# Performance work log

Hardware: AMD Instinct MI355X
Metric: run time of the kernel (lower is better)

The kernel has to match this reference:

```python
import jax, jax.numpy as jnp
import numpy as np

N, E_EDGES = 100000, 1600000
IN_DIM, HEADS, OUT_DIM = 128, 8, 8


def setup_inputs() -> dict:
    key = jax.random.key(0)
    ks = jax.random.split(key, 12)
    d = HEADS * OUT_DIM
    s = 1.0 / np.sqrt(IN_DIM)
    inp = {
        'x': jax.random.normal(ks[0], (N, IN_DIM), dtype=jnp.float32),
        'edge_attr': jax.random.normal(ks[1], (E_EDGES, 1), dtype=jnp.float32),
        'edge_index': jax.random.randint(ks[2], (2, E_EDGES), 0, N, dtype=jnp.int64),
        'Wq': jax.random.normal(ks[3], (IN_DIM, d), dtype=jnp.float32) * s,
        'bq': jnp.zeros((d,), dtype=jnp.float32),
        'Wk': jax.random.normal(ks[4], (IN_DIM, d), dtype=jnp.float32) * s,
        'bk': jnp.zeros((d,), dtype=jnp.float32),
        'We': jax.random.normal(ks[5], (1, d), dtype=jnp.float32),
        'be': jnp.zeros((d,), dtype=jnp.float32),
        'Wv': jax.random.normal(ks[6], (IN_DIM, d), dtype=jnp.float32) * s,
        'bv': jnp.zeros((d,), dtype=jnp.float32),
    }
    return inp


def reference(x, edge_attr, edge_index, Wq, bq, Wk, bk, We, be, Wv, bv):
    n = x.shape[0]
    # Projections, reshaped to [N, H, D] (and [E, H, D] for edge features)
    Qh = (x @ Wq + bq).reshape(n, HEADS, OUT_DIM)
    Kh = (x @ Wk + bk).reshape(n, HEADS, OUT_DIM)
    Vh = (x @ Wv + bv).reshape(n, HEADS, OUT_DIM)
    Eh = (edge_attr @ We + be).reshape(-1, HEADS, OUT_DIM)

    src = edge_index[0]
    dst = edge_index[1]
    # Per-edge score: (K[src] * Q[dst] / sqrt(D)) * E, summed over D, clamped, exp'd
    score = (Kh[src] * Qh[dst]) * (1.0 / np.sqrt(OUT_DIM)) * Eh  # [E, H, D]
    score = jnp.exp(jnp.clip(jnp.sum(score, axis=-1, keepdims=True), -5.0, 5.0))  # [E, H, 1]

    msg = Vh[src] * score  # [E, H, D]
    wV = jax.ops.segment_sum(msg, dst, num_segments=n)     # [N, H, D]
    Z = jax.ops.segment_sum(score, dst, num_segments=n)    # [N, H, 1]
    return wV / (Z + 1e-6)
```

## Files before the change

kernel.cpp:

```cpp
#include <hip/hip_runtime.h>
#include <math.h>

#define NN 100000
#define EE 1600000
#define IND 128
#define D64 64

#define BSHIFT 8
#define NBUCK 391
#define P1_TILE 3072
#define NB_P1 521

typedef __attribute__((ext_vector_type(8))) short  short8;
typedef __attribute__((ext_vector_type(4))) float  f32x4;

__device__ __forceinline__ unsigned short bf16_rne(float v) {
    unsigned int u = __float_as_uint(v);
    return (unsigned short)((u + 0x7FFFu + ((u >> 16) & 1u)) >> 16);
}

__global__ __launch_bounds__(256) void wtrans_kernel(
    const float* __restrict__ Wq, const float* __restrict__ Wk,
    const float* __restrict__ Wv,
    unsigned short* __restrict__ wt_hi, unsigned short* __restrict__ wt_lo)
{
    int idx = blockIdx.x * 256 + threadIdx.x;
    if (idx >= 192 * 128) return;
    int col = idx >> 7, k = idx & 127;
    const float* W = (col < 64) ? Wq : (col < 128) ? Wk : Wv;
    float v = W[(size_t)k * D64 + (col & 63)];
    unsigned short h = bf16_rne(v);
    float hf = __uint_as_float((unsigned int)h << 16);
    unsigned short l = bf16_rne(v - hf);
    wt_hi[idx] = h;
    wt_lo[idx] = l;
}

#define XP 132

__global__ __launch_bounds__(256) void qkv_kernel(
    const float* __restrict__ x,
    const unsigned short* __restrict__ wt_hi,
    const unsigned short* __restrict__ wt_lo,
    const float* __restrict__ bq, const float* __restrict__ bk,
    const float* __restrict__ bv,
    float* __restrict__ Qo, unsigned int* __restrict__ KVb)
{
    __shared__ unsigned short xhi[32 * XP];
    __shared__ unsigned short xlo[32 * XP];

    const int t    = threadIdx.x;
    const int wave = t >> 6;
    const int lane = t & 63;
    const int nb   = blockIdx.x * 32;

    {
        const int row = t >> 3;
        const int c   = t & 7;
        const float* xr = x + (size_t)(nb + row) * IND + c * 16;
        float4 a0 = *(const float4*)(xr);
        float4 a1 = *(const float4*)(xr + 4);
        float4 a2 = *(const float4*)(xr + 8);
        float4 a3 = *(const float4*)(xr + 12);
        float vs[16] = { a0.x, a0.y, a0.z, a0.w, a1.x, a1.y, a1.z, a1.w,
                         a2.x, a2.y, a2.z, a2.w, a3.x, a3.y, a3.z, a3.w };
        short8 h0, h1, l0, l1;
#pragma unroll
        for (int j = 0; j < 8; ++j) {
            unsigned short hb = bf16_rne(vs[j]);
            float hf = __uint_as_float((unsigned int)hb << 16);
            h0[j] = (short)hb;
            l0[j] = (short)bf16_rne(vs[j] - hf);
        }
#pragma unroll
        for (int j = 0; j < 8; ++j) {
            unsigned short hb = bf16_rne(vs[8 + j]);
            float hf = __uint_as_float((unsigned int)hb << 16);
            h1[j] = (short)hb;
            l1[j] = (short)bf16_rne(vs[8 + j] - hf);
        }
        int o0 = row * XP + c * 16;
        *(short8*)&xhi[o0]     = h0;
        *(short8*)&xhi[o0 + 8] = h1;
        *(short8*)&xlo[o0]     = l0;
        *(short8*)&xlo[o0 + 8] = l1;
    }
    __syncthreads();

    const int wcol0 = wave * 48;

    f32x4 acc[2][3];
#pragma unroll
    for (int rt = 0; rt < 2; ++rt)
#pragma unroll
        for (int ct = 0; ct < 3; ++ct)
            acc[rt][ct] = (f32x4){0.f, 0.f, 0.f, 0.f};

#pragma unroll
    for (int kt = 0; kt < 4; ++kt) {
        short8 bh[3], bl[3];
#pragma unroll
        for (int ct = 0; ct < 3; ++ct) {
            int col = wcol0 + ct * 16 + (lane & 15);
            int a = col * 128 + kt * 32 + (lane >> 4) * 8;
            bh[ct] = *(const short8*)&wt_hi[a];
            bl[ct] = *(const short8*)&wt_lo[a];
        }
        short8 ah[2], al[2];
#pragma unroll
        for (int rt = 0; rt < 2; ++rt) {
            int o2 = (rt * 16 + (lane & 15)) * XP + kt * 32 + (lane >> 4) * 8;
            ah[rt] = *(const short8*)&xhi[o2];
            al[rt] = *(const short8*)&xlo[o2];
        }
#pragma unroll
        for (int rt = 0; rt < 2; ++rt) {
#pragma unroll
            for (int ct = 0; ct < 3; ++ct) {
                acc[rt][ct] = __builtin_amdgcn_mfma_f32_16x16x32_bf16(
                    ah[rt], bh[ct], acc[rt][ct], 0, 0, 0);
                acc[rt][ct] = __builtin_amdgcn_mfma_f32_16x16x32_bf16(
                    ah[rt], bl[ct], acc[rt][ct], 0, 0, 0);
                acc[rt][ct] = __builtin_amdgcn_mfma_f32_16x16x32_bf16(
                    al[rt], bh[ct], acc[rt][ct], 0, 0, 0);
            }
        }
    }

#pragma unroll
    for (int ct = 0; ct < 3; ++ct) {
        int colbase = wcol0 + ct * 16;
        int m  = colbase >> 6;
        int lc = (colbase & 63) + (lane & 15);
        const float* bp = (m == 0) ? bq : (m == 1) ? bk : bv;
        float bias = bp[lc];
#pragma unroll
        for (int rt = 0; rt < 2; ++rt) {
#pragma unroll
            for (int reg = 0; reg < 4; ++reg) {
                int node = nb + rt * 16 + (lane >> 4) * 4 + reg;
                float val = acc[rt][ct][reg] + bias;
                size_t idx = (size_t)node * D64 + lc;
                if (m == 0) {
                    Qo[idx] = val;
                } else {
                    ((unsigned short*)KVb)[idx * 2 + (m == 1 ? 1 : 0)] = bf16_rne(val);
                }
            }
        }
    }
}

__global__ __launch_bounds__(256) void p1a_kernel(const int* __restrict__ ei,
                                                  int* __restrict__ hist)
{
    __shared__ int lh[NBUCK];
    const int t = threadIdx.x;
    for (int b = t; b < NBUCK; b += 256) lh[b] = 0;
    __syncthreads();

    const int e0 = blockIdx.x * P1_TILE;
#pragma unroll
    for (int j = 0; j < 12; ++j) {
        int e = e0 + j * 256 + t;
        if (e < EE) {
            int d = ei[EE + e];
            atomicAdd(&lh[d >> BSHIFT], 1);
        }
    }
    __syncthreads();
    for (int b = t; b < NBUCK; b += 256)
        hist[blockIdx.x * NBUCK + b] = lh[b];
}

__global__ __launch_bounds__(256) void hscanA_kernel(int* __restrict__ hist,
                                                     int* __restrict__ btot)
{
    const int b = blockIdx.x;
    const int t = threadIdx.x;
    int L[3]; int s = 0;
#pragma unroll
    for (int j = 0; j < 3; ++j) {
        int blk = t * 3 + j;
        L[j] = (blk < NB_P1) ? hist[blk * NBUCK + b] : 0;
        s += L[j];
    }
    int lane = t & 63, w = t >> 6;
    int incl = s;
    for (int o = 1; o < 64; o <<= 1) {
        int v = __shfl_up(incl, o);
        if (lane >= o) incl += v;
    }
    __shared__ int wsum[4];
    if (lane == 63) wsum[w] = incl;
    __syncthreads();
    int wbase = 0;
#pragma unroll
    for (int i = 0; i < 4; ++i) if (i < w) wbase += wsum[i];
    int run = wbase + incl - s;
#pragma unroll
    for (int j = 0; j < 3; ++j) {
        int blk = t * 3 + j;
        if (blk < NB_P1) hist[blk * NBUCK + b] = run;
        run += L[j];
    }
    if (t == 0) btot[b] = wsum[0] + wsum[1] + wsum[2] + wsum[3];
}

__global__ __launch_bounds__(256) void bscan_kernel(const int* __restrict__ btot,
                                                    int* __restrict__ bbase)
{
    const int t = threadIdx.x;
    int i0 = 2 * t, i1 = 2 * t + 1;
    int v0 = (i0 < NBUCK) ? btot[i0] : 0;
    int v1 = (i1 < NBUCK) ? btot[i1] : 0;
    int s = v0 + v1;
    int lane = t & 63, w = t >> 6;
    int incl = s;
    for (int o = 1; o < 64; o <<= 1) {
        int v = __shfl_up(incl, o);
        if (lane >= o) incl += v;
    }
    __shared__ int wsum[4];
    if (lane == 63) wsum[w] = incl;
    __syncthreads();
    int wbase = 0;
#pragma unroll
    for (int i = 0; i < 4; ++i) if (i < w) wbase += wsum[i];
    int excl = wbase + incl - s;
    if (i0 <= NBUCK) bbase[i0] = excl;
    if (i1 <= NBUCK) bbase[i1] = excl + v0;
}

__global__ __launch_bounds__(256) void p1b_kernel(const int* __restrict__ ei,
                                                  const float* __restrict__ ea,
                                                  const int* __restrict__ hist,
                                                  const int* __restrict__ bbase,
                                                  int2* __restrict__ staging)
{
    __shared__ int lr[NBUCK];
    const int t = threadIdx.x;
    for (int b = t; b < NBUCK; b += 256)
        lr[b] = hist[blockIdx.x * NBUCK + b] + bbase[b];
    __syncthreads();

    const int e0 = blockIdx.x * P1_TILE;
#pragma unroll
    for (int j = 0; j < 12; ++j) {
        int e = e0 + j * 256 + t;
        if (e < EE) {
            int s = ei[e];
            int d = ei[EE + e];
            int pos = atomicAdd(&lr[d >> BSHIFT], 1);
            staging[pos] = make_int2(s | ((d & 255) << 17), __float_as_int(ea[e]));
        }
    }
}

__global__ __launch_bounds__(256) void p2_kernel(const int2* __restrict__ staging,
                                                 const int* __restrict__ bbase,
                                                 int* __restrict__ off,
                                                 int2* __restrict__ epack)
{
    const int bucket = blockIdx.x;
    const int t      = threadIdx.x;
    const int n0     = bucket << BSHIFT;
    const int sb     = bbase[bucket];
    const int se     = bbase[bucket + 1];

    __shared__ int lcnt[256];
    __shared__ int lcur[256];
    __shared__ int wsum[4];
    lcnt[t] = 0;
    __syncthreads();

    for (int r = sb + t; r < se; r += 256)
        atomicAdd(&lcnt[(staging[r].x >> 17) & 255], 1);
    __syncthreads();

    int cnt  = lcnt[t];
    int lane = t & 63, w = t >> 6;
    int incl = cnt;
    for (int o = 1; o < 64; o <<= 1) {
        int v = __shfl_up(incl, o);
        if (lane >= o) incl += v;
    }
    if (lane == 63) wsum[w] = incl;
    __syncthreads();
    int wbase = 0;
#pragma unroll
    for (int i = 0; i < 4; ++i) if (i < w) wbase += wsum[i];
    int ov = sb + wbase + incl - cnt;

    int node = n0 + t;
    if (node <= NN) off[node] = ov;
    lcur[t] = ov;
    __syncthreads();

    for (int r = sb + t; r < se; r += 256) {
        int2 rec = staging[r];
        int dl = (rec.x >> 17) & 255;
        int pos = atomicAdd(&lcur[dl], 1);
        epack[pos] = make_int2(rec.x & 0x1FFFF, rec.y);
    }
}

__global__ __launch_bounds__(256) void attn_kernel(
    const float* __restrict__ Q, const unsigned int* __restrict__ KVb,
    const int* __restrict__ off, const int2* __restrict__ epack,
    const float* __restrict__ We, const float* __restrict__ be,
    float* __restrict__ out)
{
    const int lane = threadIdx.x & 63;
    const int node = blockIdx.x * 4 + (threadIdx.x >> 6);

    const int h  = lane & 7;
    const int es = lane >> 3;

    float wq[8], bq[8];
    {
        const float4* qp = (const float4*)&Q[(size_t)node * D64 + h * 8];
        float4 q0 = qp[0], q1 = qp[1];
        const float4* wp = (const float4*)&We[h * 8];
        float4 w0 = wp[0], w1 = wp[1];
        const float4* bp = (const float4*)&be[h * 8];
        float4 b0 = bp[0], b1 = bp[1];
        const float rs = 0.35355339059327373f;
        float qs[8] = { q0.x, q0.y, q0.z, q0.w, q1.x, q1.y, q1.z, q1.w };
        float ws[8] = { w0.x, w0.y, w0.z, w0.w, w1.x, w1.y, w1.z, w1.w };
        float bs[8] = { b0.x, b0.y, b0.z, b0.w, b1.x, b1.y, b1.z, b1.w };
#pragma unroll
        for (int d = 0; d < 8; ++d) {
            float qr = qs[d] * rs;
            wq[d] = ws[d] * qr;
            bq[d] = bs[d] * qr;
        }
    }

    const int i0 = off[node];
    const int i1 = off[node + 1];

    float acc[8];
#pragma unroll
    for (int d = 0; d < 8; ++d) acc[d] = 0.f;
    float z = 0.f;

    int i = i0;
#pragma unroll 2
    for (; i + 8 <= i1; i += 8) {
        int2 rec = epack[i + es];
        unsigned int bo = ((unsigned int)rec.x << 6) + (h << 3);
        float attr = __int_as_float(rec.y);

        uint4 wA = *(const uint4*)(KVb + bo);
        uint4 wB = *(const uint4*)(KVb + bo + 4);
        unsigned int wv[8] = { wA.x, wA.y, wA.z, wA.w, wB.x, wB.y, wB.z, wB.w };

        float tt = 0.f;
#pragma unroll
        for (int d = 0; d < 8; ++d) {
            float s  = fmaf(attr, wq[d], bq[d]);
            float kf = __uint_as_float(wv[d] & 0xFFFF0000u);
            tt = fmaf(kf, s, tt);
        }
        tt = fminf(fmaxf(tt, -5.f), 5.f);
        float sc = __expf(tt);

#pragma unroll
        for (int d = 0; d < 8; ++d) {
            float vf = __uint_as_float(wv[d] << 16);
            acc[d] = fmaf(vf, sc, acc[d]);
        }
        z += sc;
    }

    if (i < i1) {
        int  idx   = i + es;
        bool valid = idx < i1;
        int2 rec   = epack[valid ? idx : i0];
        unsigned int bo = ((unsigned int)rec.x << 6) + (h << 3);
        float attr = __int_as_float(rec.y);

        uint4 wA = *(const uint4*)(KVb + bo);
        uint4 wB = *(const uint4*)(KVb + bo + 4);
        unsigned int wv[8] = { wA.x, wA.y, wA.z, wA.w, wB.x, wB.y, wB.z, wB.w };

        float tt = 0.f;
#pragma unroll
        for (int d = 0; d < 8; ++d) {
            float s  = fmaf(attr, wq[d], bq[d]);
            float kf = __uint_as_float(wv[d] & 0xFFFF0000u);
            tt = fmaf(kf, s, tt);
        }
        tt = fminf(fmaxf(tt, -5.f), 5.f);
        float sc = __expf(tt);
        sc = valid ? sc : 0.f;

#pragma unroll
        for (int d = 0; d < 8; ++d) {
            float vf = __uint_as_float(wv[d] << 16);
            acc[d] = fmaf(vf, sc, acc[d]);
        }
        z += sc;
    }

#pragma unroll
    for (int m = 8; m <= 32; m <<= 1) {
#pragma unroll
        for (int d = 0; d < 8; ++d) acc[d] += __shfl_xor(acc[d], m);
        z += __shfl_xor(z, m);
    }

    float val = acc[0];
#pragma unroll
    for (int j = 1; j < 8; ++j)
        val = (es == j) ? acc[j] : val;

    out[(size_t)node * D64 + h * 8 + es] = val / (z + 1e-6f);
}

static inline size_t align256(size_t v) { return (v + 255) & ~(size_t)255; }

extern "C" void kernel_launch(void* const* d_in, const int* in_sizes, int n_in,
                              void* d_out, int out_size, void* d_ws, size_t ws_size,
                              hipStream_t stream)
{
    const float* x  = (const float*)d_in[0];
    const float* ea = (const float*)d_in[1];
    const int*   ei = (const int*)  d_in[2];
    const float* Wq = (const float*)d_in[3];
    const float* bq = (const float*)d_in[4];
    const float* Wk = (const float*)d_in[5];
    const float* bk = (const float*)d_in[6];
    const float* We = (const float*)d_in[7];
    const float* be = (const float*)d_in[8];
    const float* Wv = (const float*)d_in[9];
    const float* bv = (const float*)d_in[10];
    float* out = (float*)d_out;

    char* ws = (char*)d_ws;
    size_t o = 0;
    float*          Q       = (float*)(ws + o);          o += align256((size_t)NN * D64 * 4);
    unsigned int*   KVb     = (unsigned int*)(ws + o);   o += align256((size_t)NN * D64 * 4);
    int*            off     = (int*)(ws + o);            o += align256((size_t)(NN + 1) * 4);
    unsigned short* wt_hi   = (unsigned short*)(ws + o); o += align256((size_t)192 * 128 * 2);
    unsigned short* wt_lo   = (unsigned short*)(ws + o); o += align256((size_t)192 * 128 * 2);
    int*            hist    = (int*)(ws + o);            o += align256((size_t)NB_P1 * NBUCK * 4);
    int*            btot    = (int*)(ws + o);            o += align256((size_t)NBUCK * 4);
    int*            bbase   = (int*)(ws + o);            o += align256((size_t)(NBUCK + 1) * 4);
    int2*           staging = (int2*)(ws + o);           o += align256((size_t)EE * 8);
    int2*           epack   = (int2*)(ws + o);           o += align256((size_t)EE * 8);
    (void)ws_size; (void)out_size; (void)in_sizes; (void)n_in;

    wtrans_kernel<<<96, 256, 0, stream>>>(Wq, Wk, Wv, wt_hi, wt_lo);
    qkv_kernel<<<NN / 32, 256, 0, stream>>>(x, wt_hi, wt_lo, bq, bk, bv, Q, KVb);
    p1a_kernel<<<NB_P1, 256, 0, stream>>>(ei, hist);
    hscanA_kernel<<<NBUCK, 256, 0, stream>>>(hist, btot);
    bscan_kernel<<<1, 256, 0, stream>>>(btot, bbase);
    p1b_kernel<<<NB_P1, 256, 0, stream>>>(ei, ea, hist, bbase, staging);
    p2_kernel<<<NBUCK, 256, 0, stream>>>(staging, bbase, off, epack);
    attn_kernel<<<NN / 4, 256, 0, stream>>>(Q, KVb, off, epack, We, be, out);
}
```

Measured before the change: 167.1 us.

## Merge independent stages into shared launches to overlap projection and edge bucketing

The weight transpose and the destination histogram now share one launch, and the QKV projection GEMM and the edge scatter into staging share another, with each block choosing its role from blockIdx. This cuts the launch count from eight to six and lets the compute-bound projection run alongside the memory-bound edge scatter. The cost is larger combined kernels whose register and shared-memory footprint is set by the heavier QKV path, which may lower occupancy for the scatter blocks. The QKV blocks now run after the histogram scans instead of before them.

```diff
diff --git a/kernel.cpp b/kernel.cpp
--- a/kernel.cpp
+++ b/kernel.cpp
@@ -11,6 +11,9 @@
 #define P1_TILE 3072
 #define NB_P1 521
 
+#define QKV_BLOCKS 3125
+#define WT_BLOCKS 96
+
 typedef __attribute__((ext_vector_type(8))) short  short8;
 typedef __attribute__((ext_vector_type(4))) float  f32x4;
 
@@ -19,37 +22,146 @@
     return (unsigned short)((u + 0x7FFFu + ((u >> 16) & 1u)) >> 16);
 }
 
-__global__ __launch_bounds__(256) void wtrans_kernel(
+__global__ __launch_bounds__(256) void fusedA_kernel(
     const float* __restrict__ Wq, const float* __restrict__ Wk,
     const float* __restrict__ Wv,
-    unsigned short* __restrict__ wt_hi, unsigned short* __restrict__ wt_lo)
-{
-    int idx = blockIdx.x * 256 + threadIdx.x;
-    if (idx >= 192 * 128) return;
-    int col = idx >> 7, k = idx & 127;
-    const float* W = (col < 64) ? Wq : (col < 128) ? Wk : Wv;
-    float v = W[(size_t)k * D64 + (col & 63)];
-    unsigned short h = bf16_rne(v);
-    float hf = __uint_as_float((unsigned int)h << 16);
-    unsigned short l = bf16_rne(v - hf);
-    wt_hi[idx] = h;
-    wt_lo[idx] = l;
+    unsigned short* __restrict__ wt_hi, unsigned short* __restrict__ wt_lo,
+    const int* __restrict__ ei, int* __restrict__ hist)
+{
+    __shared__ int lh[NBUCK];
+    const int t = threadIdx.x;
+
+    if (blockIdx.x < WT_BLOCKS) {
+        int idx = blockIdx.x * 256 + t;
+        int col = idx >> 7, k = idx & 127;
+        const float* W = (col < 64) ? Wq : (col < 128) ? Wk : Wv;
+        float v = W[(size_t)k * D64 + (col & 63)];
+        unsigned short h = bf16_rne(v);
+        float hf = __uint_as_float((unsigned int)h << 16);
+        unsigned short l = bf16_rne(v - hf);
+        wt_hi[idx] = h;
+        wt_lo[idx] = l;
+        return;
+    }
+
+    const int pb = blockIdx.x - WT_BLOCKS;
+    for (int b = t; b < NBUCK; b += 256) lh[b] = 0;
+    __syncthreads();
+
+    const int e0 = pb * P1_TILE;
+#pragma unroll
+    for (int j = 0; j < 12; ++j) {
+        int e = e0 + j * 256 + t;
+        if (e < EE) {
+            int d = ei[EE + e];
+            atomicAdd(&lh[d >> BSHIFT], 1);
+        }
+    }
+    __syncthreads();
+    for (int b = t; b < NBUCK; b += 256)
+        hist[pb * NBUCK + b] = lh[b];
+}
+
+__global__ __launch_bounds__(256) void hscanA_kernel(int* __restrict__ hist,
+                                                     int* __restrict__ btot)
+{
+    const int b = blockIdx.x;
+    const int t = threadIdx.x;
+    int L[3]; int s = 0;
+#pragma unroll
+    for (int j = 0; j < 3; ++j) {
+        int blk = t * 3 + j;
+        L[j] = (blk < NB_P1) ? hist[blk * NBUCK + b] : 0;
+        s += L[j];
+    }
+    int lane = t & 63, w = t >> 6;
+    int incl = s;
+    for (int o = 1; o < 64; o <<= 1) {
+        int v = __shfl_up(incl, o);
+        if (lane >= o) incl += v;
+    }
+    __shared__ int wsum[4];
+    if (lane == 63) wsum[w] = incl;
+    __syncthreads();
+    int wbase = 0;
+#pragma unroll
+    for (int i = 0; i < 4; ++i) if (i < w) wbase += wsum[i];
+    int run = wbase + incl - s;
+#pragma unroll
+    for (int j = 0; j < 3; ++j) {
+        int blk = t * 3 + j;
+        if (blk < NB_P1) hist[blk * NBUCK + b] = run;
+        run += L[j];
+    }
+    if (t == 0) btot[b] = wsum[0] + wsum[1] + wsum[2] + wsum[3];
+}
+
+__global__ __launch_bounds__(256) void bscan_kernel(const int* __restrict__ btot,
+                                                    int* __restrict__ bbase)
+{
+    const int t = threadIdx.x;
+    int i0 = 2 * t, i1 = 2 * t + 1;
+    int v0 = (i0 < NBUCK) ? btot[i0] : 0;
+    int v1 = (i1 < NBUCK) ? btot[i1] : 0;
+    int s = v0 + v1;
+    int lane = t & 63, w = t >> 6;
+    int incl = s;
+    for (int o = 1; o < 64; o <<= 1) {
+        int v = __shfl_up(incl, o);
+        if (lane >= o) incl += v;
+    }
+    __shared__ int wsum[4];
+    if (lane == 63) wsum[w] = incl;
+    __syncthreads();
+    int wbase = 0;
+#pragma unroll
+    for (int i = 0; i < 4; ++i) if (i < w) wbase += wsum[i];
+    int excl = wbase + incl - s;
+    if (i0 <= NBUCK) bbase[i0] = excl;
+    if (i1 <= NBUCK) bbase[i1] = excl + v0;
 }
 
 #define XP 132
 
-__global__ __launch_bounds__(256) void qkv_kernel(
+__global__ __launch_bounds__(256) void fusedB_kernel(
     const float* __restrict__ x,
     const unsigned short* __restrict__ wt_hi,
     const unsigned short* __restrict__ wt_lo,
     const float* __restrict__ bq, const float* __restrict__ bk,
     const float* __restrict__ bv,
-    float* __restrict__ Qo, unsigned int* __restrict__ KVb)
-{
-    __shared__ unsigned short xhi[32 * XP];
-    __shared__ unsigned short xlo[32 * XP];
-
-    const int t    = threadIdx.x;
+    float* __restrict__ Qo, unsigned int* __restrict__ KVb,
+    const int* __restrict__ ei, const float* __restrict__ ea,
+    const int* __restrict__ hist, const int* __restrict__ bbase,
+    int2* __restrict__ staging)
+{
+    __shared__ __align__(16) char smem[2 * 32 * XP * 2];
+
+    const int t = threadIdx.x;
+
+    if (blockIdx.x >= QKV_BLOCKS) {
+        int* lr = (int*)smem;
+        const int pb = blockIdx.x - QKV_BLOCKS;
+        for (int b = t; b < NBUCK; b += 256)
+            lr[b] = hist[pb * NBUCK + b] + bbase[b];
+        __syncthreads();
+
+        const int e0 = pb * P1_TILE;
+#pragma unroll
+        for (int j = 0; j < 12; ++j) {
+            int e = e0 + j * 256 + t;
+            if (e < EE) {
+                int s = ei[e];
+                int d = ei[EE + e];
+                int pos = atomicAdd(&lr[d >> BSHIFT], 1);
+                staging[pos] = make_int2(s | ((d & 255) << 17), __float_as_int(ea[e]));
+            }
+        }
+        return;
+    }
+
+    unsigned short* xhi = (unsigned short*)smem;
+    unsigned short* xlo = (unsigned short*)(smem + 32 * XP * 2);
+
     const int wave = t >> 6;
     const int lane = t & 63;
     const int nb   = blockIdx.x * 32;
@@ -147,112 +259,6 @@
                     ((unsigned short*)KVb)[idx * 2 + (m == 1 ? 1 : 0)] = bf16_rne(val);
                 }
             }
-        }
-    }
-}
-
-__global__ __launch_bounds__(256) void p1a_kernel(const int* __restrict__ ei,
-                                                  int* __restrict__ hist)
-{
-    __shared__ int lh[NBUCK];
-    const int t = threadIdx.x;
-    for (int b = t; b < NBUCK; b += 256) lh[b] = 0;
-    __syncthreads();
-
-    const int e0 = blockIdx.x * P1_TILE;
-#pragma unroll
-    for (int j = 0; j < 12; ++j) {
-        int e = e0 + j * 256 + t;
-        if (e < EE) {
-            int d = ei[EE + e];
-            atomicAdd(&lh[d >> BSHIFT], 1);
-        }
-    }
-    __syncthreads();
-    for (int b = t; b < NBUCK; b += 256)
-        hist[blockIdx.x * NBUCK + b] = lh[b];
-}
-
-__global__ __launch_bounds__(256) void hscanA_kernel(int* __restrict__ hist,
-                                                     int* __restrict__ btot)
-{
-    const int b = blockIdx.x;
-    const int t = threadIdx.x;
-    int L[3]; int s = 0;
-#pragma unroll
-    for (int j = 0; j < 3; ++j) {
-        int blk = t * 3 + j;
-        L[j] = (blk < NB_P1) ? hist[blk * NBUCK + b] : 0;
-        s += L[j];
-    }
-    int lane = t & 63, w = t >> 6;
-    int incl = s;
-    for (int o = 1; o < 64; o <<= 1) {
-        int v = __shfl_up(incl, o);
-        if (lane >= o) incl += v;
-    }
-    __shared__ int wsum[4];
-    if (lane == 63) wsum[w] = incl;
-    __syncthreads();
-    int wbase = 0;
-#pragma unroll
-    for (int i = 0; i < 4; ++i) if (i < w) wbase += wsum[i];
-    int run = wbase + incl - s;
-#pragma unroll
-    for (int j = 0; j < 3; ++j) {
-        int blk = t * 3 + j;
-        if (blk < NB_P1) hist[blk * NBUCK + b] = run;
-        run += L[j];
-    }
-    if (t == 0) btot[b] = wsum[0] + wsum[1] + wsum[2] + wsum[3];
-}
-
-__global__ __launch_bounds__(256) void bscan_kernel(const int* __restrict__ btot,
-                                                    int* __restrict__ bbase)
-{
-    const int t = threadIdx.x;
-    int i0 = 2 * t, i1 = 2 * t + 1;
-    int v0 = (i0 < NBUCK) ? btot[i0] : 0;
-    int v1 = (i1 < NBUCK) ? btot[i1] : 0;
-    int s = v0 + v1;
-    int lane = t & 63, w = t >> 6;
-    int incl = s;
-    for (int o = 1; o < 64; o <<= 1) {
-        int v = __shfl_up(incl, o);
-        if (lane >= o) incl += v;
-    }
-    __shared__ int wsum[4];
-    if (lane == 63) wsum[w] = incl;
-    __syncthreads();
-    int wbase = 0;
-#pragma unroll
-    for (int i = 0; i < 4; ++i) if (i < w) wbase += wsum[i];
-    int excl = wbase + incl - s;
-    if (i0 <= NBUCK) bbase[i0] = excl;
-    if (i1 <= NBUCK) bbase[i1] = excl + v0;
-}
-
-__global__ __launch_bounds__(256) void p1b_kernel(const int* __restrict__ ei,
-                                                  const float* __restrict__ ea,
-                                                  const int* __restrict__ hist,
-                                                  const int* __restrict__ bbase,
-                                                  int2* __restrict__ staging)
-{
-    __shared__ int lr[NBUCK];
-    const int t = threadIdx.x;
-    for (int b = t; b < NBUCK; b += 256)
-        lr[b] = hist[blockIdx.x * NBUCK + b] + bbase[b];
-    __syncthreads();
-
-    const int e0 = blockIdx.x * P1_TILE;
-#pragma unroll
-    for (int j = 0; j < 12; ++j) {
-        int e = e0 + j * 256 + t;
-        if (e < EE) {
-            int s = ei[e];
-            int d = ei[EE + e];
-            int pos = atomicAdd(&lr[d >> BSHIFT], 1);
-            staging[pos] = make_int2(s | ((d & 255) << 17), __float_as_int(ea[e]));
         }
     }
 }
@@ -452,12 +458,11 @@
     int2*           epack   = (int2*)(ws + o);           o += align256((size_t)EE * 8);
     (void)ws_size; (void)out_size; (void)in_sizes; (void)n_in;
 
-    wtrans_kernel<<<96, 256, 0, stream>>>(Wq, Wk, Wv, wt_hi, wt_lo);
-    qkv_kernel<<<NN / 32, 256, 0, stream>>>(x, wt_hi, wt_lo, bq, bk, bv, Q, KVb);
-    p1a_kernel<<<NB_P1, 256, 0, stream>>>(ei, hist);
+    fusedA_kernel<<<WT_BLOCKS + NB_P1, 256, 0, stream>>>(Wq, Wk, Wv, wt_hi, wt_lo, ei, hist);
     hscanA_kernel<<<NBUCK, 256, 0, stream>>>(hist, btot);
     bscan_kernel<<<1, 256, 0, stream>>>(btot, bbase);
-    p1b_kernel<<<NB_P1, 256, 0, stream>>>(ei, ea, hist, bbase, staging);
+    fusedB_kernel<<<QKV_BLOCKS + NB_P1, 256, 0, stream>>>(x, wt_hi, wt_lo, bq, bk, bv,
+                                                          Q, KVb, ei, ea, hist, bbase, staging);
     p2_kernel<<<NBUCK, 256, 0, stream>>>(staging, bbase, off, epack);
     attn_kernel<<<NN / 4, 256, 0, stream>>>(Q, KVb, off, epack, We, be, out);
 }
```

New measurement: 156.1 us. 6.6% less time.
